# Kernel optimization log

Hardware: AMD Instinct MI355X
Metric: run time of the kernel (lower is better)

## Reference

```python
import jax, jax.numpy as jnp
import numpy as np
from math import factorial

P = 3          # polynomial order
D_I = 4096     # sketch output dim per order
C = 512        # input channels
B, H, W = 8, 28, 28
GAMMA = 1e-4


def setup_inputs() -> dict:
    key = jax.random.key(0)
    k1, k2, k3 = jax.random.split(key, 3)
    x = jax.random.normal(k1, (B, H, W, C), dtype=jnp.float32)
    # AlphaInitializer: alpha_i = sqrt(exp(-2g) * (2g)^i / i!)
    gam2 = np.full(P + 1, 2.0 * GAMMA)
    numer = np.power(gam2, np.arange(P + 1))
    denom = np.array([factorial(i) for i in range(P + 1)], dtype=np.float64)
    alpha = jnp.asarray(np.sqrt(np.exp(-gam2) * numer / denom), dtype=jnp.float32)
    # count-sketch hash indices and sign bits, one pair per order t in [0, p)
    h_idx = jax.random.randint(k2, (P, C), 0, D_I)
    s_bits = jax.random.randint(k3, (P, C), 0, 2).astype(jnp.int32)
    return {"x": x, "alpha": alpha, "h_idx": h_idx, "s_bits": s_bits}


def reference(x, alpha, h_idx, s_bits):
    Bs, Hs, Ws, Ch = x.shape
    p = h_idx.shape[0]
    d_i = D_I
    signs = (2 * s_bits - 1).astype(x.dtype)          # (p, C) in {-1,+1}
    x_flat = x.reshape(-1, Ch)                        # (B*H*W, C)

    def count_sketch(h, s):
        # scatter-add channels into d_i buckets: equivalent to x_flat @ S
        return jnp.zeros((x_flat.shape[0], d_i), x.dtype).at[:, h].add(x_flat * s)

    sk = jax.vmap(count_sketch)(h_idx, signs)         # (p, N, d_i)
    xs = jnp.transpose(sk, (1, 0, 2)).reshape(Bs, Hs * Ws, p, d_i)

    xf = jnp.fft.fft(xs.astype(jnp.complex64), axis=-1)
    cp = jnp.cumprod(xf, axis=-2)[:, :, 1:, :]        # orders 2..p
    xi = jnp.real(jnp.fft.ifft(cp, axis=-1)).mean(axis=1)   # (B, p-1, d_i)

    x_p = xi * alpha[2:].reshape(1, p - 1, 1)
    zeroth = alpha[0] * jnp.ones((Bs, 1), x.dtype)
    first = alpha[1] * x.mean(axis=(1, 2))            # (B, C)
    phi = jnp.concatenate([zeroth, first, x_p.reshape(Bs, -1)], axis=-1)
    phi = jnp.sign(phi) * jnp.sqrt(jnp.abs(phi) + 1e-12)    # signed sqrt
    return phi / jnp.linalg.norm(phi, axis=-1, keepdims=True)
```

## Files before the change

### kernel.cpp

```cpp
#include <hip/hip_runtime.h>

#define BATCH 8
#define NPOS 784
#define CH 512
#define DI 4096
#define PPC 14
#define CHUNKS (NPOS / PPC)
#define PHI_LEN 8705
#define S_FLOATS (BATCH * 2 * 2049 * 2)
#define PHI_OFF S_FLOATS

__device__ __forceinline__ float2 cmul(float2 a, float2 b) {
  return make_float2(a.x * b.x - a.y * b.y, a.x * b.y + a.y * b.x);
}
__device__ __forceinline__ float2 f2add(float2 a, float2 b) {
  return make_float2(a.x + b.x, a.y + b.y);
}
__device__ __forceinline__ float2 f2sub(float2 a, float2 b) {
  return make_float2(a.x - b.x, a.y - b.y);
}

__device__ __forceinline__ void dft4(float2& a, float2& b, float2& c, float2& d) {
  float t0x = a.x + c.x, t0y = a.y + c.y;
  float t1x = a.x - c.x, t1y = a.y - c.y;
  float t2x = b.x + d.x, t2y = b.y + d.y;
  float t3x = b.x - d.x, t3y = b.y - d.y;
  a = make_float2(t0x + t2x, t0y + t2y);
  c = make_float2(t0x - t2x, t0y - t2y);
  b = make_float2(t1x + t3y, t1y - t3x);
  d = make_float2(t1x - t3y, t1y + t3x);
}

__device__ __forceinline__ void dft8(float2 v[8]) {
  float2 e0 = v[0], e1 = v[2], e2 = v[4], e3 = v[6];
  dft4(e0, e1, e2, e3);
  float2 o0 = v[1], o1 = v[3], o2 = v[5], o3 = v[7];
  dft4(o0, o1, o2, o3);
  const float r = 0.70710678118654752f;
  o1 = make_float2(r * (o1.x + o1.y), r * (o1.y - o1.x));
  o2 = make_float2(o2.y, -o2.x);
  o3 = make_float2(r * (o3.y - o3.x), -r * (o3.x + o3.y));
  v[0] = f2add(e0, o0); v[4] = f2sub(e0, o0);
  v[1] = f2add(e1, o1); v[5] = f2sub(e1, o1);
  v[2] = f2add(e2, o2); v[6] = f2sub(e2, o2);
  v[3] = f2add(e3, o3); v[7] = f2sub(e3, o3);
}

__device__ __forceinline__ void twiddle8(float2 v[8], float2 w) {
  float2 w2 = cmul(w, w);
  float2 w3 = cmul(w2, w);
  float2 w4 = cmul(w2, w2);
  v[1] = cmul(v[1], w);
  v[2] = cmul(v[2], w2);
  v[3] = cmul(v[3], w3);
  v[4] = cmul(v[4], w4);
  v[5] = cmul(v[5], cmul(w4, w));
  v[6] = cmul(v[6], cmul(w4, w2));
  v[7] = cmul(v[7], cmul(w4, w3));
}

__device__ __forceinline__ void fft_stages8(float2* Z, int t, float2 w1b,
                                            float2 w2b, float2 w3b) {
  __syncthreads();
  {
    const int base = t << 3;
    const int mask0 = (t >> 1) & 15;
    float2 v[8];
    #pragma unroll
    for (int u = 0; u < 8; ++u) v[u] = Z[(base + u) ^ mask0];
    dft8(v);
    #pragma unroll
    for (int k = 0; k < 8; ++k) Z[(base + k) ^ mask0] = v[k];
  }
  __syncthreads();
  {
    const int base = ((t >> 3) << 6) + (t & 7);
    const int g4 = (t >> 3) << 2;
    float2 v[8];
    #pragma unroll
    for (int u = 0; u < 8; ++u)
      v[u] = Z[(base + (u << 3)) ^ ((g4 + (u >> 1)) & 15)];
    twiddle8(v, w1b);
    dft8(v);
    #pragma unroll
    for (int k = 0; k < 8; ++k)
      Z[(base + (k << 3)) ^ ((g4 + (k >> 1)) & 15)] = v[k];
  }
  __syncthreads();
  {
    const int base = ((t >> 6) << 9) + (t & 63);
    const int jh = (t & 63) >> 4;
    float2 v[8];
    #pragma unroll
    for (int u = 0; u < 8; ++u)
      v[u] = Z[(base + (u << 6)) ^ (((u << 2) + jh) & 15)];
    twiddle8(v, w2b);
    dft8(v);
    #pragma unroll
    for (int k = 0; k < 8; ++k)
      Z[(base + (k << 6)) ^ (((k << 2) + jh) & 15)] = v[k];
  }
  __syncthreads();
  {
    const int mask3 = (t >> 4) & 15;
    float2 v[8];
    #pragma unroll
    for (int u = 0; u < 8; ++u) v[u] = Z[(t + (u << 9)) ^ mask3];
    twiddle8(v, w3b);
    dft8(v);
    #pragma unroll
    for (int k = 0; k < 8; ++k) Z[(t + (k << 9)) ^ mask3] = v[k];
  }
  __syncthreads();
}

__global__ __launch_bounds__(512) void cbp_stage1(
    const float* __restrict__ x, const float* __restrict__ alpha,
    const int* __restrict__ h_idx, const int* __restrict__ s_bits,
    float* __restrict__ ws) {
  __shared__ float2 Z[DI];
  float* Zf = (float*)Z;
  const int t = threadIdx.x;
  const int bb = blockIdx.x / CHUNKS;
  const int ch = blockIdx.x % CHUNKS;

  auto mapq = [](int h, int s) {
    int r = ((h & 7) << 9) | (((h >> 3) & 7) << 6) | (((h >> 6) & 7) << 3) |
            (h >> 9);
    return (r ^ ((r >> 4) & 15)) | ((s ^ 1) << 31);
  };
  auto sgn = [](float v, int p) {
    return __int_as_float(__float_as_int(v) ^ ((unsigned)p & 0x80000000u));
  };
  const int q0 = mapq(h_idx[t], s_bits[t]);
  const int q1 = mapq(h_idx[CH + t], s_bits[CH + t]);
  const int q2 = mapq(h_idx[2 * CH + t], s_bits[2 * CH + t]);

  float sv_, cv_;
  __sincosf(-9.8174770424681038e-2f * (float)(t & 7), &sv_, &cv_);
  const float2 w1b = make_float2(cv_, sv_);
  __sincosf(-1.2271846303085130e-2f * (float)(t & 63), &sv_, &cv_);
  const float2 w2b = make_float2(cv_, sv_);
  __sincosf(-1.5339807878856412e-3f * (float)t, &sv_, &cv_);
  const float2 w3b = make_float2(cv_, sv_);

  const int mask3 = (t >> 4) & 15;

  float2 acc2[4], acc3[4], carry[4];
  #pragma unroll
  for (int j = 0; j < 4; ++j) {
    acc2[j] = make_float2(0.f, 0.f);
    acc3[j] = make_float2(0.f, 0.f);
  }
  float acc2x = 0.f, acc3x = 0.f, carryx = 0.f;
  float xs = 0.f;

  #pragma unroll
  for (int q = 0; q < 8; ++q) Z[t + (q << 9)] = make_float2(0.f, 0.f);
  __syncthreads();

  for (int ip = 0; ip < PPC / 2; ++ip) {
    const int n0 = bb * NPOS + ch * PPC + ip * 2;
    const float xv0 = x[(size_t)n0 * CH + t];
    const float xv1 = x[(size_t)(n0 + 1) * CH + t];
    xs += xv0 + xv1;

    atomicAdd(&Zf[2 * (q0 & 0xFFF)], sgn(xv0, q0));
    atomicAdd(&Zf[2 * (q1 & 0xFFF) + 1], sgn(xv0, q1));
    fft_stages8(Z, t, w1b, w2b, w3b);
    #pragma unroll
    for (int jj = 0; jj < 4; ++jj) {
      const int k = t + (jj << 9);
      const int ak = k ^ mask3;
      const int m = (DI - k) & (DI - 1);
      const int am = m ^ ((m >> 4) & 15);
      float2 Zk = Z[ak], Zm = Z[am];
      Z[ak] = make_float2(0.f, 0.f);
      Z[am] = make_float2(0.f, 0.f);
      float2 E = make_float2(0.5f * (Zk.x + Zm.x), 0.5f * (Zk.y - Zm.y));
      float2 O = make_float2(0.5f * (Zk.y + Zm.y), -0.5f * (Zk.x - Zm.x));
      float2 P = cmul(E, O);
      carry[jj] = P;
      acc2[jj].x += P.x;
      acc2[jj].y += P.y;
    }
    if (t == 0) {
      float2 Zq = Z[2048];
      Z[2048] = make_float2(0.f, 0.f);
      carryx = Zq.x * Zq.y;
      acc2x += carryx;
    }
    __syncthreads();

    atomicAdd(&Zf[2 * (q2 & 0xFFF)], sgn(xv0, q2));
    atomicAdd(&Zf[2 * (q0 & 0xFFF) + 1], sgn(xv1, q0));
    fft_stages8(Z, t, w1b, w2b, w3b);
    #pragma unroll
    for (int jj = 0; jj < 4; ++jj) {
      const int k = t + (jj << 9);
      const int ak = k ^ mask3;
      const int m = (DI - k) & (DI - 1);
      const int am = m ^ ((m >> 4) & 15);
      float2 Zk = Z[ak], Zm = Z[am];
      Z[ak] = make_float2(0.f, 0.f);
      Z[am] = make_float2(0.f, 0.f);
      float2 E = make_float2(0.5f * (Zk.x + Zm.x), 0.5f * (Zk.y - Zm.y));
      float2 O = make_float2(0.5f * (Zk.y + Zm.y), -0.5f * (Zk.x - Zm.x));
      float2 P3 = cmul(carry[jj], E);
      acc3[jj].x += P3.x;
      acc3[jj].y += P3.y;
      carry[jj] = O;
    }
    if (t == 0) {
      float2 Zq = Z[2048];
      Z[2048] = make_float2(0.f, 0.f);
      acc3x += carryx * Zq.x;
      carryx = Zq.y;
    }
    __syncthreads();

    atomicAdd(&Zf[2 * (q1 & 0xFFF)], sgn(xv1, q1));
    atomicAdd(&Zf[2 * (q2 & 0xFFF) + 1], sgn(xv1, q2));
    fft_stages8(Z, t, w1b, w2b, w3b);
    #pragma unroll
    for (int jj = 0; jj < 4; ++jj) {
      const int k = t + (jj << 9);
      const int ak = k ^ mask3;
      const int m = (DI - k) & (DI - 1);
      const int am = m ^ ((m >> 4) & 15);
      float2 Zk = Z[ak], Zm = Z[am];
      Z[ak] = make_float2(0.f, 0.f);
      Z[am] = make_float2(0.f, 0.f);
      float2 E = make_float2(0.5f * (Zk.x + Zm.x), 0.5f * (Zk.y - Zm.y));
      float2 O = make_float2(0.5f * (Zk.y + Zm.y), -0.5f * (Zk.x - Zm.x));
      float2 P = cmul(carry[jj], E);
      acc2[jj].x += P.x;
      acc2[jj].y += P.y;
      float2 P3 = cmul(P, O);
      acc3[jj].x += P3.x;
      acc3[jj].y += P3.y;
    }
    if (t == 0) {
      float2 Zq = Z[2048];
      Z[2048] = make_float2(0.f, 0.f);
      float tt = carryx * Zq.x;
      acc2x += tt;
      acc3x += tt * Zq.y;
    }
    __syncthreads();
  }

  float* S = ws;
  #pragma unroll
  for (int jj = 0; jj < 4; ++jj) {
    const int k = t + (jj << 9);
    float* p2p = S + ((size_t)(bb * 2 + 0) * 2049 + k) * 2;
    atomicAdd(p2p, acc2[jj].x);
    atomicAdd(p2p + 1, acc2[jj].y);
    float* p3p = S + ((size_t)(bb * 2 + 1) * 2049 + k) * 2;
    atomicAdd(p3p, acc3[jj].x);
    atomicAdd(p3p + 1, acc3[jj].y);
  }
  if (t == 0) {
    atomicAdd(S + ((size_t)(bb * 2 + 0) * 2049 + 2048) * 2, acc2x);
    atomicAdd(S + ((size_t)(bb * 2 + 1) * 2049 + 2048) * 2, acc3x);
  }

  const float sc1 = alpha[1] * (1.0f / (float)NPOS);
  float* phi = ws + PHI_OFF;
  atomicAdd(&phi[(size_t)bb * PHI_LEN + 1 + t], xs * sc1);
}

__device__ inline void fft4096_r2(float2* Z, const float2* W, int tid) {
  for (int s = 1; s <= 12; ++s) {
    __syncthreads();
    const int half = 1 << (s - 1);
    const int tsh = 12 - s;
    #pragma unroll
    for (int q = 0; q < 8; ++q) {
      int bidx = tid + q * 256;
      int j = bidx & (half - 1);
      int i1 = ((bidx >> (s - 1)) << s) + j;
      int i2 = i1 + half;
      float2 w = W[j << tsh];
      float2 u = Z[i1];
      float2 v = Z[i2];
      float2 t = cmul(w, v);
      Z[i1] = make_float2(u.x + t.x, u.y + t.y);
      Z[i2] = make_float2(u.x - t.x, u.y - t.y);
    }
  }
  __syncthreads();
}

__global__ __launch_bounds__(256) void cbp_stage2(
    const float* __restrict__ ws_in, const float* __restrict__ alpha,
    float* __restrict__ ws_phi) {
  __shared__ float2 Z[DI];
  __shared__ float2 W[DI / 2];
  const int tid = threadIdx.x;

  for (int r = tid; r < DI / 2; r += 256) {
    float ang = 1.5339807878856412e-3f * (float)r;
    float sv, cv;
    sincosf(ang, &sv, &cv);
    W[r] = make_float2(cv, sv);
  }

  const int b = blockIdx.x >> 1;
  const int t = blockIdx.x & 1;
  const float* Sp = ws_in + (size_t)(b * 2 + t) * 2049 * 2;

  for (int k = tid; k <= 2048; k += 256) {
    float re = Sp[k * 2];
    float im = Sp[k * 2 + 1];
    Z[__brev((unsigned)k) >> 20] = make_float2(re, im);
    if (k > 0 && k < 2048) {
      Z[__brev((unsigned)(DI - k)) >> 20] = make_float2(re, -im);
    }
  }
  fft4096_r2(Z, W, tid);

  const float scale = alpha[2 + t] / ((float)DI * (float)NPOS);
  float* out = ws_phi + (size_t)b * PHI_LEN + 513 + t * DI;
  for (int d = tid; d < DI; d += 256) out[d] = Z[d].x * scale;
}

__global__ __launch_bounds__(256) void cbp_stage3(
    const float* __restrict__ ws_phi, const float* __restrict__ alpha,
    float* __restrict__ out) {
  __shared__ float red[4];
  const int b = blockIdx.x;
  const int tid = threadIdx.x;
  const float* pr = ws_phi + (size_t)b * PHI_LEN;
  const float a0 = alpha[0];

  float w[35];
  float ssum = 0.f;
  #pragma unroll
  for (int j = 0; j < 35; ++j) {
    const int idx = tid + j * 256;
    float wv = 0.f;
    if (idx < PHI_LEN) {
      float v = (idx == 0) ? a0 : pr[idx];
      float sq = sqrtf(fabsf(v) + 1e-12f);
      wv = (v > 0.f) ? sq : ((v < 0.f) ? -sq : 0.f);
    }
    w[j] = wv;
    ssum += wv * wv;
  }
  for (int off = 32; off > 0; off >>= 1) ssum += __shfl_down(ssum, off);
  if ((tid & 63) == 0) red[tid >> 6] = ssum;
  __syncthreads();
  const float tot = red[0] + red[1] + red[2] + red[3];
  const float inv = 1.0f / sqrtf(tot);

  #pragma unroll
  for (int j = 0; j < 35; ++j) {
    const int idx = tid + j * 256;
    if (idx < PHI_LEN) out[(size_t)b * PHI_LEN + idx] = w[j] * inv;
  }
}

extern "C" void kernel_launch(void* const* d_in, const int* in_sizes, int n_in,
                              void* d_out, int out_size, void* d_ws,
                              size_t ws_size, hipStream_t stream) {
  const float* x = (const float*)d_in[0];
  const float* alpha = (const float*)d_in[1];
  const int* h_idx = (const int*)d_in[2];
  const int* s_bits = (const int*)d_in[3];
  float* out = (float*)d_out;
  float* ws = (float*)d_ws;

  const size_t zero_bytes = (size_t)(S_FLOATS + BATCH * PHI_LEN) * sizeof(float);
  hipMemsetAsync(d_ws, 0, zero_bytes, stream);

  cbp_stage1<<<dim3(BATCH * CHUNKS), dim3(512), 0, stream>>>(x, alpha, h_idx,
                                                             s_bits, ws);
  cbp_stage2<<<dim3(BATCH * 2), dim3(256), 0, stream>>>(ws, alpha,
                                                        ws + PHI_OFF);
  cbp_stage3<<<dim3(BATCH), dim3(256), 0, stream>>>(ws + PHI_OFF, alpha, out);
}
```

Before: 210.5 us.

## Process two position pairs per iteration with dual shared FFT buffers

Adds a second 4096-entry complex shared buffer so two independent position pairs are sketched and FFT'd together, halving the number of barriers per position. Each FFT stage runs on both buffers between syncs. Twiddles are now recomputed with sincos inside each stage to free registers. Chunk size drops from 14 to 8 positions, which doubles shared memory per block (lower occupancy), changes the block count and adds per-stage transcendental work.

Result: slower. 241.7 us (+14.8%).

```diff
diff --git a/kernel.cpp b/kernel.cpp
--- a/kernel.cpp
+++ b/kernel.cpp
@@ -4,7 +4,7 @@
 #define NPOS 784
 #define CH 512
 #define DI 4096
-#define PPC 14
+#define PPC 8
 #define CHUNKS (NPOS / PPC)
 #define PHI_LEN 8705
 #define S_FLOATS (BATCH * 2 * 2049 * 2)
@@ -59,67 +59,110 @@
   v[7] = cmul(v[7], cmul(w4, w3));
 }
 
-__device__ __forceinline__ void fft_stages8(float2* Z, int t, float2 w1b,
-                                            float2 w2b, float2 w3b) {
-  __syncthreads();
-  {
-    const int base = t << 3;
-    const int mask0 = (t >> 1) & 15;
-    float2 v[8];
-    #pragma unroll
-    for (int u = 0; u < 8; ++u) v[u] = Z[(base + u) ^ mask0];
-    dft8(v);
-    #pragma unroll
-    for (int k = 0; k < 8; ++k) Z[(base + k) ^ mask0] = v[k];
-  }
-  __syncthreads();
-  {
-    const int base = ((t >> 3) << 6) + (t & 7);
-    const int g4 = (t >> 3) << 2;
-    float2 v[8];
-    #pragma unroll
-    for (int u = 0; u < 8; ++u)
-      v[u] = Z[(base + (u << 3)) ^ ((g4 + (u >> 1)) & 15)];
-    twiddle8(v, w1b);
-    dft8(v);
-    #pragma unroll
-    for (int k = 0; k < 8; ++k)
-      Z[(base + (k << 3)) ^ ((g4 + (k >> 1)) & 15)] = v[k];
-  }
-  __syncthreads();
-  {
-    const int base = ((t >> 6) << 9) + (t & 63);
-    const int jh = (t & 63) >> 4;
-    float2 v[8];
-    #pragma unroll
-    for (int u = 0; u < 8; ++u)
-      v[u] = Z[(base + (u << 6)) ^ (((u << 2) + jh) & 15)];
-    twiddle8(v, w2b);
-    dft8(v);
-    #pragma unroll
-    for (int k = 0; k < 8; ++k)
-      Z[(base + (k << 6)) ^ (((k << 2) + jh) & 15)] = v[k];
-  }
-  __syncthreads();
-  {
-    const int mask3 = (t >> 4) & 15;
-    float2 v[8];
-    #pragma unroll
-    for (int u = 0; u < 8; ++u) v[u] = Z[(t + (u << 9)) ^ mask3];
-    twiddle8(v, w3b);
-    dft8(v);
-    #pragma unroll
-    for (int k = 0; k < 8; ++k) Z[(t + (k << 9)) ^ mask3] = v[k];
-  }
-  __syncthreads();
+__device__ __forceinline__ void fstage0(float2* Z, int t) {
+  const int base = t << 3;
+  const int mask0 = (t >> 1) & 15;
+  float2 v[8];
+  #pragma unroll
+  for (int u = 0; u < 8; ++u) v[u] = Z[(base + u) ^ mask0];
+  dft8(v);
+  #pragma unroll
+  for (int k = 0; k < 8; ++k) Z[(base + k) ^ mask0] = v[k];
+}
+__device__ __forceinline__ void fstage1(float2* Z, int t) {
+  const int base = ((t >> 3) << 6) + (t & 7);
+  const int g4 = (t >> 3) << 2;
+  float sv_, cv_;
+  __sincosf(-9.8174770424681038e-2f * (float)(t & 7), &sv_, &cv_);
+  const float2 w1b = make_float2(cv_, sv_);
+  float2 v[8];
+  #pragma unroll
+  for (int u = 0; u < 8; ++u)
+    v[u] = Z[(base + (u << 3)) ^ ((g4 + (u >> 1)) & 15)];
+  twiddle8(v, w1b);
+  dft8(v);
+  #pragma unroll
+  for (int k = 0; k < 8; ++k)
+    Z[(base + (k << 3)) ^ ((g4 + (k >> 1)) & 15)] = v[k];
+}
+__device__ __forceinline__ void fstage2(float2* Z, int t) {
+  const int base = ((t >> 6) << 9) + (t & 63);
+  const int jh = (t & 63) >> 4;
+  float sv_, cv_;
+  __sincosf(-1.2271846303085130e-2f * (float)(t & 63), &sv_, &cv_);
+  const float2 w2b = make_float2(cv_, sv_);
+  float2 v[8];
+  #pragma unroll
+  for (int u = 0; u < 8; ++u)
+    v[u] = Z[(base + (u << 6)) ^ (((u << 2) + jh) & 15)];
+  twiddle8(v, w2b);
+  dft8(v);
+  #pragma unroll
+  for (int k = 0; k < 8; ++k)
+    Z[(base + (k << 6)) ^ (((k << 2) + jh) & 15)] = v[k];
+}
+__device__ __forceinline__ void fstage3(float2* Z, int t) {
+  const int mask3 = (t >> 4) & 15;
+  float sv_, cv_;
+  __sincosf(-1.5339807878856412e-3f * (float)t, &sv_, &cv_);
+  const float2 w3b = make_float2(cv_, sv_);
+  float2 v[8];
+  #pragma unroll
+  for (int u = 0; u < 8; ++u) v[u] = Z[(t + (u << 9)) ^ mask3];
+  twiddle8(v, w3b);
+  dft8(v);
+  #pragma unroll
+  for (int k = 0; k < 8; ++k) Z[(t + (k << 9)) ^ mask3] = v[k];
+}
+
+template <int MODE>
+__device__ __forceinline__ void product_phase(
+    float2* Z, int t, float2 carry[4], float2 acc2[4], float2 acc3[4],
+    float& carryx, float& acc2x, float& acc3x) {
+  const int mask3 = (t >> 4) & 15;
+  #pragma unroll
+  for (int jj = 0; jj < 4; ++jj) {
+    const int k = t + (jj << 9);
+    const int ak = k ^ mask3;
+    const int m = (DI - k) & (DI - 1);
+    const int am = m ^ ((m >> 4) & 15);
+    float2 Zk = Z[ak], Zm = Z[am];
+    Z[ak] = make_float2(0.f, 0.f);
+    Z[am] = make_float2(0.f, 0.f);
+    float2 E = make_float2(0.5f * (Zk.x + Zm.x), 0.5f * (Zk.y - Zm.y));
+    float2 O = make_float2(0.5f * (Zk.y + Zm.y), -0.5f * (Zk.x - Zm.x));
+    if (MODE == 0) {
+      float2 P = cmul(E, O);
+      carry[jj] = P;
+      acc2[jj].x += P.x; acc2[jj].y += P.y;
+    } else if (MODE == 1) {
+      float2 P3 = cmul(carry[jj], E);
+      acc3[jj].x += P3.x; acc3[jj].y += P3.y;
+      carry[jj] = O;
+    } else {
+      float2 P = cmul(carry[jj], E);
+      acc2[jj].x += P.x; acc2[jj].y += P.y;
+      float2 P3 = cmul(P, O);
+      acc3[jj].x += P3.x; acc3[jj].y += P3.y;
+    }
+  }
+  if (t == 0) {
+    float2 Zq = Z[2048];
+    Z[2048] = make_float2(0.f, 0.f);
+    if (MODE == 0) { carryx = Zq.x * Zq.y; acc2x += carryx; }
+    else if (MODE == 1) { acc3x += carryx * Zq.x; carryx = Zq.y; }
+    else { float tt = carryx * Zq.x; acc2x += tt; acc3x += tt * Zq.y; }
+  }
 }
 
 __global__ __launch_bounds__(512) void cbp_stage1(
     const float* __restrict__ x, const float* __restrict__ alpha,
     const int* __restrict__ h_idx, const int* __restrict__ s_bits,
     float* __restrict__ ws) {
-  __shared__ float2 Z[DI];
-  float* Zf = (float*)Z;
+  __shared__ float2 ZA[DI];
+  __shared__ float2 ZB[DI];
+  float* ZAf = (float*)ZA;
+  float* ZBf = (float*)ZB;
   const int t = threadIdx.x;
   const int bb = blockIdx.x / CHUNKS;
   const int ch = blockIdx.x % CHUNKS;
@@ -136,117 +179,67 @@
   const int q1 = mapq(h_idx[CH + t], s_bits[CH + t]);
   const int q2 = mapq(h_idx[2 * CH + t], s_bits[2 * CH + t]);
 
-  float sv_, cv_;
-  __sincosf(-9.8174770424681038e-2f * (float)(t & 7), &sv_, &cv_);
-  const float2 w1b = make_float2(cv_, sv_);
-  __sincosf(-1.2271846303085130e-2f * (float)(t & 63), &sv_, &cv_);
-  const float2 w2b = make_float2(cv_, sv_);
-  __sincosf(-1.5339807878856412e-3f * (float)t, &sv_, &cv_);
-  const float2 w3b = make_float2(cv_, sv_);
-
-  const int mask3 = (t >> 4) & 15;
-
-  float2 acc2[4], acc3[4], carry[4];
+  float2 acc2[4], acc3[4], carryA[4], carryB[4];
   #pragma unroll
   for (int j = 0; j < 4; ++j) {
     acc2[j] = make_float2(0.f, 0.f);
     acc3[j] = make_float2(0.f, 0.f);
   }
-  float acc2x = 0.f, acc3x = 0.f, carryx = 0.f;
+  float acc2x = 0.f, acc3x = 0.f, carryxA = 0.f, carryxB = 0.f;
   float xs = 0.f;
 
   #pragma unroll
-  for (int q = 0; q < 8; ++q) Z[t + (q << 9)] = make_float2(0.f, 0.f);
+  for (int q = 0; q < 8; ++q) {
+    ZA[t + (q << 9)] = make_float2(0.f, 0.f);
+    ZB[t + (q << 9)] = make_float2(0.f, 0.f);
+  }
   __syncthreads();
 
-  for (int ip = 0; ip < PPC / 2; ++ip) {
-    const int n0 = bb * NPOS + ch * PPC + ip * 2;
-    const float xv0 = x[(size_t)n0 * CH + t];
-    const float xv1 = x[(size_t)(n0 + 1) * CH + t];
-    xs += xv0 + xv1;
-
-    atomicAdd(&Zf[2 * (q0 & 0xFFF)], sgn(xv0, q0));
-    atomicAdd(&Zf[2 * (q1 & 0xFFF) + 1], sgn(xv0, q1));
-    fft_stages8(Z, t, w1b, w2b, w3b);
-    #pragma unroll
-    for (int jj = 0; jj < 4; ++jj) {
-      const int k = t + (jj << 9);
-      const int ak = k ^ mask3;
-      const int m = (DI - k) & (DI - 1);
-      const int am = m ^ ((m >> 4) & 15);
-      float2 Zk = Z[ak], Zm = Z[am];
-      Z[ak] = make_float2(0.f, 0.f);
-      Z[am] = make_float2(0.f, 0.f);
-      float2 E = make_float2(0.5f * (Zk.x + Zm.x), 0.5f * (Zk.y - Zm.y));
-      float2 O = make_float2(0.5f * (Zk.y + Zm.y), -0.5f * (Zk.x - Zm.x));
-      float2 P = cmul(E, O);
-      carry[jj] = P;
-      acc2[jj].x += P.x;
-      acc2[jj].y += P.y;
-    }
-    if (t == 0) {
-      float2 Zq = Z[2048];
-      Z[2048] = make_float2(0.f, 0.f);
-      carryx = Zq.x * Zq.y;
-      acc2x += carryx;
-    }
-    __syncthreads();
-
-    atomicAdd(&Zf[2 * (q2 & 0xFFF)], sgn(xv0, q2));
-    atomicAdd(&Zf[2 * (q0 & 0xFFF) + 1], sgn(xv1, q0));
-    fft_stages8(Z, t, w1b, w2b, w3b);
-    #pragma unroll
-    for (int jj = 0; jj < 4; ++jj) {
-      const int k = t + (jj << 9);
-      const int ak = k ^ mask3;
-      const int m = (DI - k) & (DI - 1);
-      const int am = m ^ ((m >> 4) & 15);
-      float2 Zk = Z[ak], Zm = Z[am];
-      Z[ak] = make_float2(0.f, 0.f);
-      Z[am] = make_float2(0.f, 0.f);
-      float2 E = make_float2(0.5f * (Zk.x + Zm.x), 0.5f * (Zk.y - Zm.y));
-      float2 O = make_float2(0.5f * (Zk.y + Zm.y), -0.5f * (Zk.x - Zm.x));
-      float2 P3 = cmul(carry[jj], E);
-      acc3[jj].x += P3.x;
-      acc3[jj].y += P3.y;
-      carry[jj] = O;
-    }
-    if (t == 0) {
-      float2 Zq = Z[2048];
-      Z[2048] = make_float2(0.f, 0.f);
-      acc3x += carryx * Zq.x;
-      carryx = Zq.y;
-    }
-    __syncthreads();
-
-    atomicAdd(&Zf[2 * (q1 & 0xFFF)], sgn(xv1, q1));
-    atomicAdd(&Zf[2 * (q2 & 0xFFF) + 1], sgn(xv1, q2));
-    fft_stages8(Z, t, w1b, w2b, w3b);
-    #pragma unroll
-    for (int jj = 0; jj < 4; ++jj) {
-      const int k = t + (jj << 9);
-      const int ak = k ^ mask3;
-      const int m = (DI - k) & (DI - 1);
-      const int am = m ^ ((m >> 4) & 15);
-      float2 Zk = Z[ak], Zm = Z[am];
-      Z[ak] = make_float2(0.f, 0.f);
-      Z[am] = make_float2(0.f, 0.f);
-      float2 E = make_float2(0.5f * (Zk.x + Zm.x), 0.5f * (Zk.y - Zm.y));
-      float2 O = make_float2(0.5f * (Zk.y + Zm.y), -0.5f * (Zk.x - Zm.x));
-      float2 P = cmul(carry[jj], E);
-      acc2[jj].x += P.x;
-      acc2[jj].y += P.y;
-      float2 P3 = cmul(P, O);
-      acc3[jj].x += P3.x;
-      acc3[jj].y += P3.y;
-    }
-    if (t == 0) {
-      float2 Zq = Z[2048];
-      Z[2048] = make_float2(0.f, 0.f);
-      float tt = carryx * Zq.x;
-      acc2x += tt;
-      acc3x += tt * Zq.y;
-    }
+  for (int ip = 0; ip < PPC / 4; ++ip) {
+    const int n0 = bb * NPOS + ch * PPC + ip * 4;
+    const float a0 = x[(size_t)n0 * CH + t];
+    const float a1 = x[(size_t)(n0 + 1) * CH + t];
+    const float b0 = x[(size_t)(n0 + 2) * CH + t];
+    const float b1 = x[(size_t)(n0 + 3) * CH + t];
+    xs += a0 + a1 + b0 + b1;
+
+    atomicAdd(&ZAf[2 * (q0 & 0xFFF)], sgn(a0, q0));
+    atomicAdd(&ZAf[2 * (q1 & 0xFFF) + 1], sgn(a0, q1));
+    atomicAdd(&ZBf[2 * (q0 & 0xFFF)], sgn(b0, q0));
+    atomicAdd(&ZBf[2 * (q1 & 0xFFF) + 1], sgn(b0, q1));
+    __syncthreads();
+    fstage0(ZA, t); fstage0(ZB, t); __syncthreads();
+    fstage1(ZA, t); fstage1(ZB, t); __syncthreads();
+    fstage2(ZA, t); fstage2(ZB, t); __syncthreads();
+    fstage3(ZA, t); fstage3(ZB, t); __syncthreads();
+    product_phase<0>(ZA, t, carryA, acc2, acc3, carryxA, acc2x, acc3x);
+    product_phase<0>(ZB, t, carryB, acc2, acc3, carryxB, acc2x, acc3x);
+    __syncthreads();
+
+    atomicAdd(&ZAf[2 * (q2 & 0xFFF)], sgn(a0, q2));
+    atomicAdd(&ZAf[2 * (q0 & 0xFFF) + 1], sgn(a1, q0));
+    atomicAdd(&ZBf[2 * (q2 & 0xFFF)], sgn(b0, q2));
+    atomicAdd(&ZBf[2 * (q0 & 0xFFF) + 1], sgn(b1, q0));
+    __syncthreads();
+    fstage0(ZA, t); fstage0(ZB, t); __syncthreads();
+    fstage1(ZA, t); fstage1(ZB, t); __syncthreads();
+    fstage2(ZA, t); fstage2(ZB, t); __syncthreads();
+    fstage3(ZA, t); fstage3(ZB, t); __syncthreads();
+    product_phase<1>(ZA, t, carryA, acc2, acc3, carryxA, acc2x, acc3x);
+    product_phase<1>(ZB, t, carryB, acc2, acc3, carryxB, acc2x, acc3x);
+    __syncthreads();
+
+    atomicAdd(&ZAf[2 * (q1 & 0xFFF)], sgn(a1, q1));
+    atomicAdd(&ZAf[2 * (q2 & 0xFFF) + 1], sgn(a1, q2));
+    atomicAdd(&ZBf[2 * (q1 & 0xFFF)], sgn(b1, q1));
+    atomicAdd(&ZBf[2 * (q2 & 0xFFF) + 1], sgn(b1, q2));
+    __syncthreads();
+    fstage0(ZA, t); fstage0(ZB, t); __syncthreads();
+    fstage1(ZA, t); fstage1(ZB, t); __syncthreads();
+    fstage2(ZA, t); fstage2(ZB, t); __syncthreads();
+    fstage3(ZA, t); fstage3(ZB, t); __syncthreads();
+    product_phase<2>(ZA, t, carryA, acc2, acc3, carryxA, acc2x, acc3x);
+    product_phase<2>(ZB, t, carryB, acc2, acc3, carryxB, acc2x, acc3x);
     __syncthreads();
   }
 
```
